# Kernel optimization log

Hardware: AMD Instinct MI355X
Metric: run time of the kernel (lower is better)

The kernel has to match this reference:

```python
import jax, jax.numpy as jnp
import numpy as np

B, N, C_Z, H, C_H, W = 1, 192, 128, 4, 32, 16


def _layer_norm(x, w, b, eps=1e-5):
    mu = jnp.mean(x, axis=-1, keepdims=True)
    var = jnp.mean(jnp.square(x - mu), axis=-1, keepdims=True)
    return (x - mu) * jax.lax.rsqrt(var + eps) * w + b


def setup_inputs() -> dict:
    key = jax.random.key(0)
    ks = jax.random.split(key, 10)
    s = 0.02
    return {
        "z": jax.random.normal(ks[0], (B, N, N, C_Z), jnp.float32),
        "mask": jnp.ones((B, N, N), jnp.float32),
        "ln_w": jnp.ones((C_Z,), jnp.float32),
        "ln_b": jnp.zeros((C_Z,), jnp.float32),
        "w_q": jax.random.normal(ks[1], (C_Z, H * C_H), jnp.float32) * s,
        "w_k": jax.random.normal(ks[2], (C_Z, H * C_H), jnp.float32) * s,
        "w_v": jax.random.normal(ks[3], (C_Z, H * C_H), jnp.float32) * s,
        "w_bias": jax.random.normal(ks[4], (C_Z, H), jnp.float32) * s,
        "w_gate": jax.random.normal(ks[5], (C_Z, H * C_H), jnp.float32) * s,
        "b_gate": jnp.ones((H * C_H,), jnp.float32),
        "w_out": jax.random.normal(ks[6], (H * C_H, C_Z), jnp.float32) * s,
        "b_out": jnp.zeros((C_Z,), jnp.float32),
        "window_size": W,
    }


def reference(z, mask, ln_w, ln_b, w_q, w_k, w_v, w_bias, w_gate, b_gate, w_out, b_out, window_size):
    b, n = z.shape[0], z.shape[1]
    h = w_bias.shape[1]
    c = w_q.shape[1] // h
    w = int(window_size)

    zl = _layer_norm(z, ln_w, ln_b)                       # [B,N,N,Cz]
    q = (zl @ w_q).reshape(b, n, n, h, c)                 # [B,I,J,H,c]
    k = (zl @ w_k).reshape(b, n, n, h, c)
    v = (zl @ w_v).reshape(b, n, n, h, c)
    tb = zl @ w_bias                                      # [B,J,K,H] triangle bias

    # sliding window indices along the key axis, centered at each query j
    idx = jnp.arange(n)[:, None] - (w // 2) + jnp.arange(w)[None, :]   # [N,W]
    valid = (idx >= 0) & (idx < n)                                     # [N,W]
    idx_c = jnp.clip(idx, 0, n - 1)

    k_win = k[:, :, idx_c]                                # [B,I,J,W,H,c]
    v_win = v[:, :, idx_c]                                # [B,I,J,W,H,c]
    tb_win = jnp.take_along_axis(tb, idx_c[None, :, :, None], axis=2)  # [B,J,W,H]
    mask_win = mask[:, :, idx_c] * valid[None, None].astype(mask.dtype)  # [B,I,J,W]

    scale = 1.0 / jnp.sqrt(jnp.asarray(c, z.dtype))
    logits = jnp.einsum('bijhc,bijwhc->bijwh', q * scale, k_win)       # [B,I,J,W,H]
    logits = logits + tb_win[:, None]                                  # bias b_{j,k} broadcast over i
    logits = logits + jnp.where(mask_win > 0, 0.0, -1e9)[..., None]
    attn = jax.nn.softmax(logits, axis=3)

    o = jnp.einsum('bijwh,bijwhc->bijhc', attn, v_win)                 # [B,I,J,H,c]
    g = jax.nn.sigmoid(zl @ w_gate + b_gate).reshape(b, n, n, h, c)
    o = (g * o).reshape(b, n, n, h * c)
    return o @ w_out + b_out                                           # [B,I,J,Cz]
```

## Files before the change

### kernel.cpp

```cpp
#include <hip/hip_runtime.h>
#include <hip/hip_bf16.h>

#define N 192
#define CZ 128
#define NH 4
#define CH 32
#define WIN 16
#define NROWS (N*N)

typedef __attribute__((ext_vector_type(8))) short bf16x8;
typedef __attribute__((ext_vector_type(4))) float f32x4;

static __device__ __forceinline__ ushort f2bf(float x){
    union{float f; unsigned u;} a; a.f = x;
    unsigned r = a.u + 0x7fffu + ((a.u>>16)&1u);
    return (ushort)(r>>16);
}
static __device__ __forceinline__ float bf2f(ushort s){
    union{unsigned u; float f;} a; a.u = ((unsigned)s)<<16;
    return a.f;
}

__global__ __launch_bounds__(256) void k_pack(
    const float* __restrict__ wq, const float* __restrict__ wk,
    const float* __restrict__ wv, const float* __restrict__ wg,
    const float* __restrict__ wo, ushort* __restrict__ WP)
{
    const int m = blockIdx.y;
    const float* W = (m==0)?wq:(m==1)?wk:(m==2)?wv:(m==3)?wg:wo;
    const int f = blockIdx.x*256 + threadIdx.x;
    const int nt = f >> 8, ks = (f >> 6) & 3, lane8 = f & 63;
    const int col = nt*16 + (lane8 & 15);
    const int r0  = ks*32 + (lane8 >> 4)*8;
    ushort tmp[8];
    #pragma unroll
    for (int i=0; i<8; i++) tmp[i] = f2bf(W[(size_t)(r0+i)*CZ + col]);
    *(uint4*)(WP + (size_t)m*16384 + (size_t)f*8) = *(uint4*)tmp;
}

__global__ __launch_bounds__(256) void k_tb(
    const float* __restrict__ z, const float* __restrict__ lnw, const float* __restrict__ lnb,
    const float* __restrict__ wbias, float* __restrict__ tb)
{
    const int tid = threadIdx.x;
    const int wave = tid >> 6, lane = tid & 63;
    const int r  = wave*4 + (lane >> 4);
    const int li = lane & 15;
    const int row = blockIdx.x*16 + r;
    const float* zr = z + (size_t)row*CZ + li*8;
    float4 a = ((const float4*)zr)[0];
    float4 b = ((const float4*)zr)[1];
    float s  = a.x+a.y+a.z+a.w + b.x+b.y+b.z+b.w;
    float s2 = a.x*a.x+a.y*a.y+a.z*a.z+a.w*a.w + b.x*b.x+b.y*b.y+b.z*b.z+b.w*b.w;
    #pragma unroll
    for (int off=1; off<16; off<<=1) { s += __shfl_xor(s, off); s2 += __shfl_xor(s2, off); }
    const float mu   = s * (1.f/CZ);
    const float rstd = rsqrtf(s2*(1.f/CZ) - mu*mu + 1e-5f);
    const int c0 = li*8;
    float vals[8] = {a.x,a.y,a.z,a.w,b.x,b.y,b.z,b.w};
    float tbp[4] = {0.f,0.f,0.f,0.f};
    #pragma unroll
    for (int t=0; t<8; t++) {
        const float nv = (vals[t]-mu)*rstd*lnw[c0+t] + lnb[c0+t];
        float4 wb4 = *(const float4*)(wbias + (c0+t)*4);
        tbp[0] += nv*wb4.x; tbp[1] += nv*wb4.y;
        tbp[2] += nv*wb4.z; tbp[3] += nv*wb4.w;
    }
    #pragma unroll
    for (int off=1; off<16; off<<=1) {
        #pragma unroll
        for (int h=0; h<4; h++) tbp[h] += __shfl_xor(tbp[h], off);
    }
    if (li == 0) *(float4*)(tb + (size_t)row*4) = make_float4(tbp[0],tbp[1],tbp[2],tbp[3]);
}

__global__ __launch_bounds__(256, 2) void k_fused(
    const float* __restrict__ z, const float* __restrict__ lnw, const float* __restrict__ lnb,
    const float* __restrict__ mask, const float* __restrict__ tb,
    const ushort* __restrict__ WP, const float* __restrict__ bg,
    const float* __restrict__ bout, float* __restrict__ out)
{
    __shared__ ushort zlds[48][132];
    __shared__ ushort kl[48][NH][40];
    __shared__ ushort vl[48][NH][40];
    __shared__ ushort qb[32][136];
    __shared__ ushort gb[32][136];
    __shared__ float  ml[48];
    ushort (*po)[136] = (ushort (*)[136])&zlds[0][0];

    const int i   = blockIdx.y;
    const int j0  = blockIdx.x * 32;
    const int tid = threadIdx.x;
    const int wid = tid >> 6, lane = tid & 63;
    const int l16 = lane & 15, lk = lane >> 4;

    for (int it = 0; it < 3; ++it) {
        const int r   = it*16 + wid*4 + lk;
        const int jj  = j0 - 8 + r;
        const int jjc = min(max(jj, 0), N-1);
        const float* zr = z + ((size_t)i*N + jjc)*CZ + l16*8;
        float4 a = ((const float4*)zr)[0];
        float4 b = ((const float4*)zr)[1];
        float s  = a.x+a.y+a.z+a.w + b.x+b.y+b.z+b.w;
        float s2 = a.x*a.x+a.y*a.y+a.z*a.z+a.w*a.w + b.x*b.x+b.y*b.y+b.z*b.z+b.w*b.w;
        #pragma unroll
        for (int off=1; off<16; off<<=1) { s += __shfl_xor(s, off); s2 += __shfl_xor(s2, off); }
        const float mu   = s * (1.f/CZ);
        const float rstd = rsqrtf(s2*(1.f/CZ) - mu*mu + 1e-5f);
        const int c0 = l16*8;
        float vals[8] = {a.x,a.y,a.z,a.w,b.x,b.y,b.z,b.w};
        uint4 pk; ushort* ph = (ushort*)&pk;
        #pragma unroll
        for (int t=0; t<8; t++)
            ph[t] = f2bf((vals[t]-mu)*rstd*lnw[c0+t] + lnb[c0+t]);
        *(uint4*)&zlds[r][c0] = pk;
    }
    if (tid < 47) {
        const int jj  = j0 - 8 + tid;
        const int jjc = min(max(jj, 0), N-1);
        const bool ok = (jj >= 0) && (jj < N) && (mask[(size_t)i*N + jjc] > 0.f);
        ml[tid] = ok ? 0.f : -1e9f;
    }
    __syncthreads();

    #pragma unroll 1
    for (int m = 1; m <= 2; ++m) {
        bf16x8 bfrag[2][4];
        #pragma unroll
        for (int nt2=0; nt2<2; nt2++)
            #pragma unroll
            for (int ks=0; ks<4; ks++)
                bfrag[nt2][ks] = *(const bf16x8*)(WP + (size_t)m*16384 + (wid*2+nt2)*2048 + ks*512 + lane*8);
        ushort (*dst)[NH][40] = (m==1) ? kl : vl;
        #pragma unroll
        for (int t=0; t<3; ++t) {
            const int slot0 = t*16;
            bf16x8 af[4];
            #pragma unroll
            for (int ks=0; ks<4; ks++)
                af[ks] = *(const bf16x8*)&zlds[slot0 + l16][ks*32 + lk*8];
            #pragma unroll
            for (int nt2=0; nt2<2; nt2++) {
                f32x4 acc = {0.f,0.f,0.f,0.f};
                #pragma unroll
                for (int ks=0; ks<4; ks++)
                    acc = __builtin_amdgcn_mfma_f32_16x16x32_bf16(bfrag[nt2][ks], af[ks], acc, 0, 0, 0);
                uint2 pk2;
                pk2.x = (unsigned)f2bf(acc[0]) | ((unsigned)f2bf(acc[1])<<16);
                pk2.y = (unsigned)f2bf(acc[2]) | ((unsigned)f2bf(acc[3])<<16);
                *(uint2*)&dst[slot0 + l16][wid][nt2*16 + lk*4] = pk2;
            }
        }
    }
    {
        #pragma unroll 1
        for (int mm = 0; mm < 2; ++mm) {
            const int m = mm ? 3 : 0;
            bf16x8 bfrag[2][4];
            float4 bg4[2];
            #pragma unroll
            for (int nt2=0; nt2<2; nt2++) {
                #pragma unroll
                for (int ks=0; ks<4; ks++)
                    bfrag[nt2][ks] = *(const bf16x8*)(WP + (size_t)m*16384 + (wid*2+nt2)*2048 + ks*512 + lane*8);
                if (mm) bg4[nt2] = *(const float4*)(bg + wid*32 + nt2*16 + lk*4);
            }
            #pragma unroll
            for (int t=0; t<2; ++t) {
                const int slot0 = 8 + t*16;
                bf16x8 af[4];
                #pragma unroll
                for (int ks=0; ks<4; ks++)
                    af[ks] = *(const bf16x8*)&zlds[slot0 + l16][ks*32 + lk*8];
                #pragma unroll
                for (int nt2=0; nt2<2; nt2++) {
                    f32x4 acc = {0.f,0.f,0.f,0.f};
                    #pragma unroll
                    for (int ks=0; ks<4; ks++)
                        acc = __builtin_amdgcn_mfma_f32_16x16x32_bf16(bfrag[nt2][ks], af[ks], acc, 0, 0, 0);
                    float v0,v1,v2,v3;
                    if (mm) {
                        v0 = 1.f/(1.f + __expf(-(acc[0] + bg4[nt2].x)));
                        v1 = 1.f/(1.f + __expf(-(acc[1] + bg4[nt2].y)));
                        v2 = 1.f/(1.f + __expf(-(acc[2] + bg4[nt2].z)));
                        v3 = 1.f/(1.f + __expf(-(acc[3] + bg4[nt2].w)));
                    } else { v0=acc[0]; v1=acc[1]; v2=acc[2]; v3=acc[3]; }
                    uint2 pk2;
                    pk2.x = (unsigned)f2bf(v0) | ((unsigned)f2bf(v1)<<16);
                    pk2.y = (unsigned)f2bf(v2) | ((unsigned)f2bf(v3)<<16);
                    if (mm) *(uint2*)&gb[t*16 + l16][wid*32 + nt2*16 + lk*4] = pk2;
                    else    *(uint2*)&qb[t*16 + l16][wid*32 + nt2*16 + lk*4] = pk2;
                }
            }
        }
    }
    __syncthreads();

    const int chalf = tid & 1;
    const int h     = (tid >> 1) & 3;
    const int jloc  = tid >> 3;
    const int j     = j0 + jloc;
    const int c0l   = chalf * 16;

    float qv[16];
    {
        uint4 q1 = *(const uint4*)&qb[jloc][h*CH + c0l];
        uint4 q2 = *(const uint4*)&qb[jloc][h*CH + c0l + 8];
        const ushort* s1 = (const ushort*)&q1;
        const ushort* s2 = (const ushort*)&q2;
        #pragma unroll
        for (int t=0; t<8; t++) { qv[t] = bf2f(s1[t]); qv[8+t] = bf2f(s2[t]); }
    }

    const float scale = 0.17677669529663688f;
    float lg[WIN];
    #pragma unroll
    for (int w=0; w<WIN; w++) {
        const int rel = jloc + w;
        float dot = 0.f;
        #pragma unroll
        for (int c4=0; c4<2; c4++) {
            uint4 kv = *(const uint4*)&kl[rel][h][c0l + c4*8];
            const ushort* kp = (const ushort*)&kv;
            #pragma unroll
            for (int t=0; t<8; t++) dot += qv[c4*8+t]*bf2f(kp[t]);
        }
        dot += __shfl_xor(dot, 1);
        const int jj  = j - 8 + w;
        const int jjc = min(max(jj, 0), N-1);
        lg[w] = dot*scale + tb[((size_t)j*N + jjc)*4 + h] + ml[rel];
    }
    float mx = lg[0];
    #pragma unroll
    for (int w=1; w<WIN; w++) mx = fmaxf(mx, lg[w]);
    float sum = 0.f;
    #pragma unroll
    for (int w=0; w<WIN; w++) { lg[w] = __expf(lg[w]-mx); sum += lg[w]; }
    const float inv = 1.f/sum;

    float o[16];
    #pragma unroll
    for (int c=0; c<16; c++) o[c] = 0.f;
    #pragma unroll
    for (int w=0; w<WIN; w++) {
        const float p   = lg[w]*inv;
        const int   rel = jloc + w;
        #pragma unroll
        for (int c4=0; c4<2; c4++) {
            uint4 vv = *(const uint4*)&vl[rel][h][c0l + c4*8];
            const ushort* vp = (const ushort*)&vv;
            #pragma unroll
            for (int t=0; t<8; t++) o[c4*8+t] += p*bf2f(vp[t]);
        }
    }

    uint4 o1, o2;
    {
        uint4 g1 = *(const uint4*)&gb[jloc][h*CH + c0l];
        uint4 g2 = *(const uint4*)&gb[jloc][h*CH + c0l + 8];
        const ushort* s1 = (const ushort*)&g1;
        const ushort* s2 = (const ushort*)&g2;
        ushort* p1 = (ushort*)&o1; ushort* p2 = (ushort*)&o2;
        #pragma unroll
        for (int t=0; t<8; t++) {
            p1[t] = f2bf(o[t]   * bf2f(s1[t]));
            p2[t] = f2bf(o[8+t] * bf2f(s2[t]));
        }
    }
    *(uint4*)&po[jloc][h*CH + c0l]     = o1;
    *(uint4*)&po[jloc][h*CH + c0l + 8] = o2;

    bf16x8 bfrag[2][4];
    float4 bo4[2];
    #pragma unroll
    for (int nt2=0; nt2<2; nt2++) {
        #pragma unroll
        for (int ks=0; ks<4; ks++)
            bfrag[nt2][ks] = *(const bf16x8*)(WP + (size_t)4*16384 + (wid*2+nt2)*2048 + ks*512 + lane*8);
        bo4[nt2] = *(const float4*)(bout + wid*32 + nt2*16 + lk*4);
    }
    __syncthreads();

    #pragma unroll
    for (int rt=0; rt<2; rt++) {
        bf16x8 af[4];
        #pragma unroll
        for (int ks=0; ks<4; ks++)
            af[ks] = *(const bf16x8*)&po[rt*16 + l16][ks*32 + lk*8];
        const size_t orow = (size_t)(i*N + j0 + rt*16 + l16)*CZ;
        #pragma unroll
        for (int nt2=0; nt2<2; nt2++) {
            f32x4 acc = {0.f,0.f,0.f,0.f};
            #pragma unroll
            for (int ks=0; ks<4; ks++)
                acc = __builtin_amdgcn_mfma_f32_16x16x32_bf16(bfrag[nt2][ks], af[ks], acc, 0, 0, 0);
            float4 ov;
            ov.x = acc[0] + bo4[nt2].x; ov.y = acc[1] + bo4[nt2].y;
            ov.z = acc[2] + bo4[nt2].z; ov.w = acc[3] + bo4[nt2].w;
            *(float4*)(out + orow + wid*32 + nt2*16 + lk*4) = ov;
        }
    }
}

extern "C" void kernel_launch(void* const* d_in, const int* in_sizes, int n_in,
                              void* d_out, int out_size, void* d_ws, size_t ws_size,
                              hipStream_t stream)
{
    const float* z    = (const float*)d_in[0];
    const float* mask = (const float*)d_in[1];
    const float* lnw  = (const float*)d_in[2];
    const float* lnb  = (const float*)d_in[3];
    const float* wq   = (const float*)d_in[4];
    const float* wk   = (const float*)d_in[5];
    const float* wv   = (const float*)d_in[6];
    const float* wb   = (const float*)d_in[7];
    const float* wg   = (const float*)d_in[8];
    const float* bg   = (const float*)d_in[9];
    const float* wo   = (const float*)d_in[10];
    const float* bo   = (const float*)d_in[11];

    float*  tb = (float*)d_ws;
    ushort* WP = (ushort*)(tb + (size_t)NROWS*4);
    if (ws_size < (size_t)NROWS*4*sizeof(float) + 5*16384*sizeof(ushort)) return;

    k_pack <<<dim3(8,5), 256, 0, stream>>>(wq, wk, wv, wg, wo, WP);
    k_tb   <<<NROWS/16, 256, 0, stream>>>(z, lnw, lnb, wb, tb);
    k_fused<<<dim3(N/32, N), 256, 0, stream>>>(z, lnw, lnb, mask, tb, WP, bg, bo, (float*)d_out);
}
```

Measured before the change: 56.29 us.

## Double fused kernel block to 512 threads and split projection work across wave halves

The fused attention kernel now runs 512 threads per block instead of 256. The layernorm load is spread over the wider block, and the K/V/Q/gate projections are load-balanced across two groups of four waves. The attention stage gives each thread 8 channels instead of 16, using an extra shuffle to reduce the dot product. The output projection assigns one row tile per wave. The aim is more parallelism and latency hiding per tile, at the cost of extra shuffles and an occupancy constraint of 4 blocks of 512 threads, which may cap registers.

```diff
diff --git a/kernel.cpp b/kernel.cpp
--- a/kernel.cpp
+++ b/kernel.cpp
@@ -74,7 +74,7 @@
     if (li == 0) *(float4*)(tb + (size_t)row*4) = make_float4(tbp[0],tbp[1],tbp[2],tbp[3]);
 }
 
-__global__ __launch_bounds__(256, 2) void k_fused(
+__global__ __launch_bounds__(512, 4) void k_fused(
     const float* __restrict__ z, const float* __restrict__ lnw, const float* __restrict__ lnb,
     const float* __restrict__ mask, const float* __restrict__ tb,
     const ushort* __restrict__ WP, const float* __restrict__ bg,
@@ -94,26 +94,30 @@
     const int wid = tid >> 6, lane = tid & 63;
     const int l16 = lane & 15, lk = lane >> 4;
 
-    for (int it = 0; it < 3; ++it) {
-        const int r   = it*16 + wid*4 + lk;
-        const int jj  = j0 - 8 + r;
-        const int jjc = min(max(jj, 0), N-1);
-        const float* zr = z + ((size_t)i*N + jjc)*CZ + l16*8;
-        float4 a = ((const float4*)zr)[0];
-        float4 b = ((const float4*)zr)[1];
-        float s  = a.x+a.y+a.z+a.w + b.x+b.y+b.z+b.w;
-        float s2 = a.x*a.x+a.y*a.y+a.z*a.z+a.w*a.w + b.x*b.x+b.y*b.y+b.z*b.z+b.w*b.w;
-        #pragma unroll
-        for (int off=1; off<16; off<<=1) { s += __shfl_xor(s, off); s2 += __shfl_xor(s2, off); }
-        const float mu   = s * (1.f/CZ);
-        const float rstd = rsqrtf(s2*(1.f/CZ) - mu*mu + 1e-5f);
-        const int c0 = l16*8;
-        float vals[8] = {a.x,a.y,a.z,a.w,b.x,b.y,b.z,b.w};
-        uint4 pk; ushort* ph = (ushort*)&pk;
-        #pragma unroll
-        for (int t=0; t<8; t++)
-            ph[t] = f2bf((vals[t]-mu)*rstd*lnw[c0+t] + lnb[c0+t]);
-        *(uint4*)&zlds[r][c0] = pk;
+    #pragma unroll
+    for (int pass = 0; pass < 2; ++pass) {
+        const int r = pass*32 + (tid >> 4);
+        if (r < 48) {
+            const int li  = tid & 15;
+            const int jj  = j0 - 8 + r;
+            const int jjc = min(max(jj, 0), N-1);
+            const float* zr = z + ((size_t)i*N + jjc)*CZ + li*8;
+            float4 a = ((const float4*)zr)[0];
+            float4 b = ((const float4*)zr)[1];
+            float s  = a.x+a.y+a.z+a.w + b.x+b.y+b.z+b.w;
+            float s2 = a.x*a.x+a.y*a.y+a.z*a.z+a.w*a.w + b.x*b.x+b.y*b.y+b.z*b.z+b.w*b.w;
+            #pragma unroll
+            for (int off=1; off<16; off<<=1) { s += __shfl_xor(s, off); s2 += __shfl_xor(s2, off); }
+            const float mu   = s * (1.f/CZ);
+            const float rstd = rsqrtf(s2*(1.f/CZ) - mu*mu + 1e-5f);
+            const int c0 = li*8;
+            float vals[8] = {a.x,a.y,a.z,a.w,b.x,b.y,b.z,b.w};
+            uint4 pk; ushort* ph = (ushort*)&pk;
+            #pragma unroll
+            for (int t=0; t<8; t++)
+                ph[t] = f2bf((vals[t]-mu)*rstd*lnw[c0+t] + lnb[c0+t]);
+            *(uint4*)&zlds[r][c0] = pk;
+        }
     }
     if (tid < 47) {
         const int jj  = j0 - 8 + tid;
@@ -123,18 +127,19 @@
     }
     __syncthreads();
 
-    #pragma unroll 1
-    for (int m = 1; m <= 2; ++m) {
+    {
+        const int cw   = wid & 3;
+        const int half = wid >> 2;
+
         bf16x8 bfrag[2][4];
-        #pragma unroll
-        for (int nt2=0; nt2<2; nt2++)
-            #pragma unroll
-            for (int ks=0; ks<4; ks++)
-                bfrag[nt2][ks] = *(const bf16x8*)(WP + (size_t)m*16384 + (wid*2+nt2)*2048 + ks*512 + lane*8);
-        ushort (*dst)[NH][40] = (m==1) ? kl : vl;
-        #pragma unroll
-        for (int t=0; t<3; ++t) {
-            const int slot0 = t*16;
+        auto loadB = [&](int m) {
+            #pragma unroll
+            for (int nt2=0; nt2<2; nt2++)
+                #pragma unroll
+                for (int ks=0; ks<4; ks++)
+                    bfrag[nt2][ks] = *(const bf16x8*)(WP + (size_t)m*16384 + (cw*2+nt2)*2048 + ks*512 + lane*8);
+        };
+        auto projKV = [&](int slot0, ushort (*dst)[NH][40]) {
             bf16x8 af[4];
             #pragma unroll
             for (int ks=0; ks<4; ks++)
@@ -148,68 +153,62 @@
                 uint2 pk2;
                 pk2.x = (unsigned)f2bf(acc[0]) | ((unsigned)f2bf(acc[1])<<16);
                 pk2.y = (unsigned)f2bf(acc[2]) | ((unsigned)f2bf(acc[3])<<16);
-                *(uint2*)&dst[slot0 + l16][wid][nt2*16 + lk*4] = pk2;
+                *(uint2*)&dst[slot0 + l16][cw][nt2*16 + lk*4] = pk2;
             }
-        }
-    }
-    {
-        #pragma unroll 1
-        for (int mm = 0; mm < 2; ++mm) {
-            const int m = mm ? 3 : 0;
-            bf16x8 bfrag[2][4];
+        };
+        auto projQG = [&](int slot0, ushort (*dst)[136], bool gate) {
             float4 bg4[2];
+            if (gate)
+                #pragma unroll
+                for (int nt2=0; nt2<2; nt2++)
+                    bg4[nt2] = *(const float4*)(bg + cw*32 + nt2*16 + lk*4);
+            bf16x8 af[4];
+            #pragma unroll
+            for (int ks=0; ks<4; ks++)
+                af[ks] = *(const bf16x8*)&zlds[slot0 + l16][ks*32 + lk*8];
             #pragma unroll
             for (int nt2=0; nt2<2; nt2++) {
+                f32x4 acc = {0.f,0.f,0.f,0.f};
                 #pragma unroll
                 for (int ks=0; ks<4; ks++)
-                    bfrag[nt2][ks] = *(const bf16x8*)(WP + (size_t)m*16384 + (wid*2+nt2)*2048 + ks*512 + lane*8);
-                if (mm) bg4[nt2] = *(const float4*)(bg + wid*32 + nt2*16 + lk*4);
+                    acc = __builtin_amdgcn_mfma_f32_16x16x32_bf16(bfrag[nt2][ks], af[ks], acc, 0, 0, 0);
+                float v0,v1,v2,v3;
+                if (gate) {
+                    v0 = 1.f/(1.f + __expf(-(acc[0] + bg4[nt2].x)));
+                    v1 = 1.f/(1.f + __expf(-(acc[1] + bg4[nt2].y)));
+                    v2 = 1.f/(1.f + __expf(-(acc[2] + bg4[nt2].z)));
+                    v3 = 1.f/(1.f + __expf(-(acc[3] + bg4[nt2].w)));
+                } else { v0=acc[0]; v1=acc[1]; v2=acc[2]; v3=acc[3]; }
+                uint2 pk2;
+                pk2.x = (unsigned)f2bf(v0) | ((unsigned)f2bf(v1)<<16);
+                pk2.y = (unsigned)f2bf(v2) | ((unsigned)f2bf(v3)<<16);
+                *(uint2*)&dst[slot0 - 8 + l16][cw*32 + nt2*16 + lk*4] = pk2;
             }
-            #pragma unroll
-            for (int t=0; t<2; ++t) {
-                const int slot0 = 8 + t*16;
-                bf16x8 af[4];
-                #pragma unroll
-                for (int ks=0; ks<4; ks++)
-                    af[ks] = *(const bf16x8*)&zlds[slot0 + l16][ks*32 + lk*8];
-                #pragma unroll
-                for (int nt2=0; nt2<2; nt2++) {
-                    f32x4 acc = {0.f,0.f,0.f,0.f};
-                    #pragma unroll
-                    for (int ks=0; ks<4; ks++)
-                        acc = __builtin_amdgcn_mfma_f32_16x16x32_bf16(bfrag[nt2][ks], af[ks], acc, 0, 0, 0);
-                    float v0,v1,v2,v3;
-                    if (mm) {
-                        v0 = 1.f/(1.f + __expf(-(acc[0] + bg4[nt2].x)));
-                        v1 = 1.f/(1.f + __expf(-(acc[1] + bg4[nt2].y)));
-                        v2 = 1.f/(1.f + __expf(-(acc[2] + bg4[nt2].z)));
-                        v3 = 1.f/(1.f + __expf(-(acc[3] + bg4[nt2].w)));
-                    } else { v0=acc[0]; v1=acc[1]; v2=acc[2]; v3=acc[3]; }
-                    uint2 pk2;
-                    pk2.x = (unsigned)f2bf(v0) | ((unsigned)f2bf(v1)<<16);
-                    pk2.y = (unsigned)f2bf(v2) | ((unsigned)f2bf(v3)<<16);
-                    if (mm) *(uint2*)&gb[t*16 + l16][wid*32 + nt2*16 + lk*4] = pk2;
-                    else    *(uint2*)&qb[t*16 + l16][wid*32 + nt2*16 + lk*4] = pk2;
-                }
-            }
+        };
+
+        if (half == 0) {
+            loadB(1); projKV(0, kl); projKV(16, kl); projKV(32, kl);
+            loadB(2); projKV(0, vl); projKV(16, vl);
+        } else {
+            loadB(2); projKV(32, vl);
+            loadB(0); projQG(8, qb, false); projQG(24, qb, false);
+            loadB(3); projQG(8, gb, true);  projQG(24, gb, true);
         }
     }
     __syncthreads();
 
-    const int chalf = tid & 1;
-    const int h     = (tid >> 1) & 3;
-    const int jloc  = tid >> 3;
-    const int j     = j0 + jloc;
-    const int c0l   = chalf * 16;
-
-    float qv[16];
+    const int cq   = tid & 3;
+    const int h    = (tid >> 2) & 3;
+    const int jloc = tid >> 4;
+    const int j    = j0 + jloc;
+    const int c0l  = cq * 8;
+
+    float qv[8];
     {
         uint4 q1 = *(const uint4*)&qb[jloc][h*CH + c0l];
-        uint4 q2 = *(const uint4*)&qb[jloc][h*CH + c0l + 8];
         const ushort* s1 = (const ushort*)&q1;
-        const ushort* s2 = (const ushort*)&q2;
-        #pragma unroll
-        for (int t=0; t<8; t++) { qv[t] = bf2f(s1[t]); qv[8+t] = bf2f(s2[t]); }
+        #pragma unroll
+        for (int t=0; t<8; t++) qv[t] = bf2f(s1[t]);
     }
 
     const float scale = 0.17677669529663688f;
@@ -218,14 +217,14 @@
     for (int w=0; w<WIN; w++) {
         const int rel = jloc + w;
         float dot = 0.f;
-        #pragma unroll
-        for (int c4=0; c4<2; c4++) {
-            uint4 kv = *(const uint4*)&kl[rel][h][c0l + c4*8];
+        {
+            uint4 kv = *(const uint4*)&kl[rel][h][c0l];
             const ushort* kp = (const ushort*)&kv;
             #pragma unroll
-            for (int t=0; t<8; t++) dot += qv[c4*8+t]*bf2f(kp[t]);
+            for (int t=0; t<8; t++) dot += qv[t]*bf2f(kp[t]);
         }
         dot += __shfl_xor(dot, 1);
+        dot += __shfl_xor(dot, 2);
         const int jj  = j - 8 + w;
         const int jjc = min(max(jj, 0), N-1);
         lg[w] = dot*scale + tb[((size_t)j*N + jjc)*4 + h] + ml[rel];
@@ -238,51 +237,42 @@
     for (int w=0; w<WIN; w++) { lg[w] = __expf(lg[w]-mx); sum += lg[w]; }
     const float inv = 1.f/sum;
 
-    float o[16];
-    #pragma unroll
-    for (int c=0; c<16; c++) o[c] = 0.f;
+    float o[8];
+    #pragma unroll
+    for (int c=0; c<8; c++) o[c] = 0.f;
     #pragma unroll
     for (int w=0; w<WIN; w++) {
         const float p   = lg[w]*inv;
         const int   rel = jloc + w;
-        #pragma unroll
-        for (int c4=0; c4<2; c4++) {
-            uint4 vv = *(const uint4*)&vl[rel][h][c0l + c4*8];
-            const ushort* vp = (const ushort*)&vv;
-            #pragma unroll
-            for (int t=0; t<8; t++) o[c4*8+t] += p*bf2f(vp[t]);
-        }
-    }
-
-    uint4 o1, o2;
+        uint4 vv = *(const uint4*)&vl[rel][h][c0l];
+        const ushort* vp = (const ushort*)&vv;
+        #pragma unroll
+        for (int t=0; t<8; t++) o[t] += p*bf2f(vp[t]);
+    }
+
     {
         uint4 g1 = *(const uint4*)&gb[jloc][h*CH + c0l];
-        uint4 g2 = *(const uint4*)&gb[jloc][h*CH + c0l + 8];
         const ushort* s1 = (const ushort*)&g1;
-        const ushort* s2 = (const ushort*)&g2;
-        ushort* p1 = (ushort*)&o1; ushort* p2 = (ushort*)&o2;
-        #pragma unroll
-        for (int t=0; t<8; t++) {
-            p1[t] = f2bf(o[t]   * bf2f(s1[t]));
-            p2[t] = f2bf(o[8+t] * bf2f(s2[t]));
-        }
-    }
-    *(uint4*)&po[jloc][h*CH + c0l]     = o1;
-    *(uint4*)&po[jloc][h*CH + c0l + 8] = o2;
-
+        uint4 o1; ushort* p1 = (ushort*)&o1;
+        #pragma unroll
+        for (int t=0; t<8; t++) p1[t] = f2bf(o[t] * bf2f(s1[t]));
+        *(uint4*)&po[jloc][h*CH + c0l] = o1;
+    }
+
+    const int rt  = wid >> 2;
+    const int cwo = wid & 3;
     bf16x8 bfrag[2][4];
     float4 bo4[2];
     #pragma unroll
     for (int nt2=0; nt2<2; nt2++) {
         #pragma unroll
         for (int ks=0; ks<4; ks++)
-            bfrag[nt2][ks] = *(const bf16x8*)(WP + (size_t)4*16384 + (wid*2+nt2)*2048 + ks*512 + lane*8);
-        bo4[nt2] = *(const float4*)(bout + wid*32 + nt2*16 + lk*4);
+            bfrag[nt2][ks] = *(const bf16x8*)(WP + (size_t)4*16384 + (cwo*2+nt2)*2048 + ks*512 + lane*8);
+        bo4[nt2] = *(const float4*)(bout + cwo*32 + nt2*16 + lk*4);
     }
     __syncthreads();
 
-    #pragma unroll
-    for (int rt=0; rt<2; rt++) {
+    {
         bf16x8 af[4];
         #pragma unroll
         for (int ks=0; ks<4; ks++)
@@ -297,7 +287,7 @@
             float4 ov;
             ov.x = acc[0] + bo4[nt2].x; ov.y = acc[1] + bo4[nt2].y;
             ov.z = acc[2] + bo4[nt2].z; ov.w = acc[3] + bo4[nt2].w;
-            *(float4*)(out + orow + wid*32 + nt2*16 + lk*4) = ov;
+            *(float4*)(out + orow + cwo*32 + nt2*16 + lk*4) = ov;
         }
     }
 }
@@ -325,5 +315,5 @@
 
     k_pack <<<dim3(8,5), 256, 0, stream>>>(wq, wk, wv, wg, wo, WP);
     k_tb   <<<NROWS/16, 256, 0, stream>>>(z, lnw, lnb, wb, tb);
-    k_fused<<<dim3(N/32, N), 256, 0, stream>>>(z, lnw, lnb, mask, tb, WP, bg, bo, (float*)d_out);
-}
+    k_fused<<<dim3(N/32, N), 512, 0, stream>>>(z, lnw, lnb, mask, tb, WP, bg, bo, (float*)d_out);
+}
```

After: 54.63 us. -2.9%, faster.
